# Kernel optimization log

Hardware: AMD Instinct MI355X
Metric: run time of the kernel (lower is better)

The kernel has to match this reference:

```python
import jax, jax.numpy as jnp
import numpy as np

RADIUS = 2  # kernel_size=5 -> r = (5-1)//2
EPS = 1e-8


def _diff(x, r, axis):
    # sliding-window sum from a cumsum along `axis` (same trick as BoxFilter.diff_x/diff_y)
    def sl(a, b):
        idx = [slice(None)] * x.ndim
        idx[axis] = slice(a, b)
        return x[tuple(idx)]
    left = sl(r, 2 * r + 1)
    middle = sl(2 * r + 1, None) - sl(None, -2 * r - 1)
    right = sl(-1, None) - sl(-2 * r - 1, -r - 1)
    return jnp.concatenate([left, middle, right], axis=axis)


def box_filter(x, r):
    # cumsum over H then window-diff, cumsum over W then window-diff
    return _diff(_diff(jnp.cumsum(x, axis=2), r, 2).cumsum(axis=3), r, 3)


def resize_bilinear_align_corners(x, out_h, out_w):
    # x: [N, C, h, w] -> [N, C, out_h, out_w], align_corners=True
    n, c, h, w = x.shape
    ys = jnp.linspace(0.0, h - 1.0, out_h, dtype=x.dtype)
    xs = jnp.linspace(0.0, w - 1.0, out_w, dtype=x.dtype)
    y0 = jnp.floor(ys).astype(jnp.int32)
    x0 = jnp.floor(xs).astype(jnp.int32)
    y1 = jnp.minimum(y0 + 1, h - 1)
    x1 = jnp.minimum(x0 + 1, w - 1)
    wy = (ys - y0.astype(x.dtype))[None, None, :, None]
    wx = (xs - x0.astype(x.dtype))[None, None, None, :]
    rows = x[:, :, y0, :] * (1 - wy) + x[:, :, y1, :] * wy  # [N,C,out_h,w]
    out = rows[:, :, :, x0] * (1 - wx) + rows[:, :, :, x1] * wx
    return out


def setup_inputs() -> dict:
    key = jax.random.key(0)
    k1, k2, k3 = jax.random.split(key, 3)
    return {
        "input_lowres": jax.random.uniform(k1, (8, 3, 256, 256), dtype=jnp.float32),
        "guide_lowres": jax.random.uniform(k2, (8, 3, 256, 256), dtype=jnp.float32),
        "input_highres": jax.random.uniform(k3, (8, 3, 1024, 1024), dtype=jnp.float32),
    }


def reference(input_lowres, guide_lowres, input_highres):
    x_lr, y_lr, x_hr = input_lowres, guide_lowres, input_highres
    r = RADIUS
    _, _, h_lr, w_lr = x_lr.shape
    _, _, h_hr, w_hr = x_hr.shape
    N = box_filter(jnp.ones((1, 1, h_lr, w_lr), dtype=x_lr.dtype), r)  # window pixel counts
    mean_x = box_filter(x_lr, r) / N
    mean_y = box_filter(y_lr, r) / N
    cov_xy = box_filter(x_lr * y_lr, r) / N - mean_x * mean_y
    var_x = box_filter(x_lr * x_lr, r) / N - mean_x * mean_x
    A = cov_xy / (var_x + EPS)
    b = mean_y - A * mean_x
    mean_A = resize_bilinear_align_corners(A, h_hr, w_hr)
    mean_b = resize_bilinear_align_corners(b, h_hr, w_hr)
    return mean_A * x_hr + mean_b
```

## Files before the change

kernel.cpp:

```cpp
#include <hip/hip_runtime.h>


typedef float f4 __attribute__((ext_vector_type(4)));

constexpr int H_LR = 256, W_LR = 256;
constexpr int H_HR = 1024, W_HR = 1024;
constexpr int NC   = 24;
constexpr int RAD  = 2;
constexpr int RPB  = 8;

constexpr int CS_W      = W_LR + 4;
constexpr int LDS_BYTES = 4 * CS_W * 4 * 4;

__global__ void __launch_bounds__(256) fgf_fused(const float* __restrict__ xlr,
                                                 const float* __restrict__ ylr,
                                                 const float* __restrict__ xhr,
                                                 float* __restrict__ out) {
    __shared__ __align__(16) char lds[LDS_BYTES];
    auto sx = reinterpret_cast<float(*)[W_LR]>(lds);
    auto sy = reinterpret_cast<float(*)[W_LR]>(lds + 8 * W_LR * 4);
    auto cs = reinterpret_cast<float(*)[CS_W][4]>(lds);
    auto ab = reinterpret_cast<float(*)[W_LR][2]>(lds);

    const int c  = blockIdx.y;
    const int i0 = blockIdx.x * RPB;
    const int t  = (int)threadIdx.x;
    const float scale = (float)(H_LR - 1) / (float)(H_HR - 1);

    const int y0min = (int)((float)i0 * scale);

    const int lrbase = c * (H_LR * W_LR);
    f4 stx[2], sty[2];
    int lr_[2], q_[2];
    #pragma unroll
    for (int half = 0; half < 2; ++half) {
        const int idx = half * 256 + t;
        lr_[half] = idx >> 6;
        q_[half]  = idx & 63;
        const int gr = y0min - 2 + lr_[half];
        f4 vx = {0.f, 0.f, 0.f, 0.f};
        f4 vy = {0.f, 0.f, 0.f, 0.f};
        if (gr >= 0 && gr < H_LR) {
            vx = *(const f4*)(xlr + lrbase + gr * W_LR + q_[half] * 4);
            vy = *(const f4*)(ylr + lrbase + gr * W_LR + q_[half] * 4);
        }
        stx[half] = vx;
        sty[half] = vy;
    }
    const size_t hrbase = ((size_t)c << 20) + (size_t)i0 * W_HR + t * 4;
    f4 xv[RPB];
    #pragma unroll
    for (int k = 0; k < RPB; ++k)
        xv[k] = *(const f4*)(xhr + hrbase + (size_t)k * W_HR);

    #pragma unroll
    for (int half = 0; half < 2; ++half) {
        *(f4*)&sx[lr_[half]][q_[half] * 4] = stx[half];
        *(f4*)&sy[lr_[half]][q_[half] * 4] = sty[half];
    }
    __syncthreads();

    float vx[8], vy[8];
    #pragma unroll
    for (int l = 0; l < 8; ++l) { vx[l] = sx[l][t]; vy[l] = sy[l][t]; }
    __syncthreads();

    #pragma unroll
    for (int rr = 0; rr < 4; ++rr) {
        float a = 0.f, b = 0.f, cxy = 0.f, cxx = 0.f;
        #pragma unroll
        for (int l = rr; l < rr + 5; ++l) {
            a += vx[l]; b += vy[l]; cxy += vx[l] * vy[l]; cxx += vx[l] * vx[l];
        }
        f4 v = {a, b, cxy, cxx};
        *(f4*)&cs[rr][t + 2][0] = v;
    }
    if (t < 2) {
        const f4 z = {0.f, 0.f, 0.f, 0.f};
        #pragma unroll
        for (int rr = 0; rr < 4; ++rr) {
            *(f4*)&cs[rr][t][0] = z;
            *(f4*)&cs[rr][t + W_LR + 2][0] = z;
        }
    }
    __syncthreads();

    const int hcnt = min(t + RAD, W_LR - 1) - max(t - RAD, 0) + 1;
    float aa[4], bb[4];
    #pragma unroll
    for (int rr = 0; rr < 4; ++rr) {
        f4 s = {0.f, 0.f, 0.f, 0.f};
        #pragma unroll
        for (int d = 0; d < 5; ++d) s += *(const f4*)&cs[rr][t + d][0];
        const int r  = y0min + rr;
        const int v0 = max(r - RAD, 0), v1 = min(r + RAD, H_LR - 1);
        const float inv = 1.0f / (float)((v1 - v0 + 1) * hcnt);
        const float mx  = s.x * inv;
        const float my  = s.y * inv;
        const float cov = s.z * inv - mx * my;
        const float var = s.w * inv - mx * mx;
        aa[rr] = cov / (var + 1e-8f);
        bb[rr] = my - aa[rr] * mx;
    }
    __syncthreads();

    #pragma unroll
    for (int rr = 0; rr < 4; ++rr) {
        ab[rr][t][0] = aa[rr];
        ab[rr][t][1] = bb[rr];
    }
    __syncthreads();

    float ax[4][4], bx[4][4];
    #pragma unroll
    for (int m = 0; m < 4; ++m) {
        const int   j   = t * 4 + m;
        const float fx  = (float)j * scale;
        const int   x0  = (int)fx;
        const float wx  = fx - (float)x0;
        const int   x1  = min(x0 + 1, W_LR - 1);
        const float wx0 = 1.f - wx;
        #pragma unroll
        for (int rr = 0; rr < 4; ++rr) {
            ax[rr][m] = ab[rr][x0][0] * wx0 + ab[rr][x1][0] * wx;
            bx[rr][m] = ab[rr][x0][1] * wx0 + ab[rr][x1][1] * wx;
        }
    }

    #pragma unroll
    for (int k = 0; k < RPB; ++k) {
        const int   i   = i0 + k;
        const float fy  = (float)i * scale;
        const int   yy0 = (int)fy;
        const float wy  = fy - (float)yy0;
        const int   l0  = yy0 - y0min;
        const int   l1  = min(yy0 + 1, H_LR - 1) - y0min;
        const float w0  = (l0 == 0 ? 1.f - wy : 0.f) + (l1 == 0 ? wy : 0.f);
        const float w1  = (l0 == 1 ? 1.f - wy : 0.f) + (l1 == 1 ? wy : 0.f);
        const float w2  = (l0 == 2 ? 1.f - wy : 0.f) + (l1 == 2 ? wy : 0.f);
        const float w3  = (l1 == 3 ? wy : 0.f);

        f4 ov;
        #pragma unroll
        for (int m = 0; m < 4; ++m) {
            const float a = ax[0][m] * w0 + ax[1][m] * w1 + ax[2][m] * w2 + ax[3][m] * w3;
            const float b = bx[0][m] * w0 + bx[1][m] * w1 + bx[2][m] * w2 + bx[3][m] * w3;
            ov[m] = a * xv[k][m] + b;
        }
        __builtin_nontemporal_store(ov, (f4*)(out + hrbase + (size_t)k * W_HR));
    }
}

extern "C" void kernel_launch(void* const* d_in, const int* in_sizes, int n_in,
                              void* d_out, int out_size, void* d_ws, size_t ws_size,
                              hipStream_t stream) {
    const float* x_lr = (const float*)d_in[0];
    const float* y_lr = (const float*)d_in[1];
    const float* x_hr = (const float*)d_in[2];
    float* out = (float*)d_out;

    dim3 grid(H_HR / RPB, NC, 1);
    fgf_fused<<<grid, 256, 0, stream>>>(x_lr, y_lr, x_hr, out);
}
```

Baseline: 41.93 us.

## Double rows per block, use sliding vertical sums, and software-pipeline high-res loads

Each block now produces 16 high-res rows from 6 low-res coefficient rows, halving the grid and cutting redundant low-res staging and box-filter work per output row. Vertical box sums use a running add/subtract window. Horizontal interpolation reads only three neighbouring A/b coefficients per thread instead of gathering per output column. High-res input loads go through a 4-deep rolling register buffer rather than all being loaded up front. The risk is fewer blocks for latency hiding and more register pressure from the larger per-thread coefficient arrays.

```diff
diff --git a/kernel.cpp b/kernel.cpp
--- a/kernel.cpp
+++ b/kernel.cpp
@@ -2,15 +2,18 @@
 
 
 typedef float f4 __attribute__((ext_vector_type(4)));
+typedef float f2 __attribute__((ext_vector_type(2)));
 
 constexpr int H_LR = 256, W_LR = 256;
 constexpr int H_HR = 1024, W_HR = 1024;
 constexpr int NC   = 24;
 constexpr int RAD  = 2;
-constexpr int RPB  = 8;
+constexpr int RPB  = 16;
+constexpr int NAB  = 6;
+constexpr int NST  = 10;
+constexpr int CS_W = W_LR + 4;
 
-constexpr int CS_W      = W_LR + 4;
-constexpr int LDS_BYTES = 4 * CS_W * 4 * 4;
+constexpr int LDS_BYTES = NAB * CS_W * 4 * 4;
 
 __global__ void __launch_bounds__(256) fgf_fused(const float* __restrict__ xlr,
                                                  const float* __restrict__ ylr,
@@ -18,9 +21,9 @@
                                                  float* __restrict__ out) {
     __shared__ __align__(16) char lds[LDS_BYTES];
     auto sx = reinterpret_cast<float(*)[W_LR]>(lds);
-    auto sy = reinterpret_cast<float(*)[W_LR]>(lds + 8 * W_LR * 4);
+    auto sy = reinterpret_cast<float(*)[W_LR]>(lds + NST * W_LR * 4);
     auto cs = reinterpret_cast<float(*)[CS_W][4]>(lds);
-    auto ab = reinterpret_cast<float(*)[W_LR][2]>(lds);
+    auto ab = reinterpret_cast<f2(*)[W_LR]>(lds);
 
     const int c  = blockIdx.y;
     const int i0 = blockIdx.x * RPB;
@@ -30,55 +33,54 @@
     const int y0min = (int)((float)i0 * scale);
 
     const int lrbase = c * (H_LR * W_LR);
-    f4 stx[2], sty[2];
-    int lr_[2], q_[2];
+    f4  stv[5];
+    int soff[5];
     #pragma unroll
-    for (int half = 0; half < 2; ++half) {
-        const int idx = half * 256 + t;
-        lr_[half] = idx >> 6;
-        q_[half]  = idx & 63;
-        const int gr = y0min - 2 + lr_[half];
-        f4 vx = {0.f, 0.f, 0.f, 0.f};
-        f4 vy = {0.f, 0.f, 0.f, 0.f};
-        if (gr >= 0 && gr < H_LR) {
-            vx = *(const f4*)(xlr + lrbase + gr * W_LR + q_[half] * 4);
-            vy = *(const f4*)(ylr + lrbase + gr * W_LR + q_[half] * 4);
-        }
-        stx[half] = vx;
-        sty[half] = vy;
+    for (int r = 0; r < 5; ++r) {
+        const int  idx = r * 256 + t;
+        const bool isx = idx < NST * 64;
+        const int  id2 = isx ? idx : idx - NST * 64;
+        const int  lr  = id2 >> 6, q = id2 & 63;
+        const int  gr  = y0min - 2 + lr;
+        const float* src = isx ? xlr : ylr;
+        f4 v = {0.f, 0.f, 0.f, 0.f};
+        if (gr >= 0 && gr < H_LR) v = *(const f4*)(src + lrbase + gr * W_LR + q * 4);
+        stv[r]  = v;
+        soff[r] = (isx ? 0 : NST * W_LR) + lr * W_LR + q * 4;
     }
-    const size_t hrbase = ((size_t)c << 20) + (size_t)i0 * W_HR + t * 4;
-    f4 xv[RPB];
-    #pragma unroll
-    for (int k = 0; k < RPB; ++k)
-        xv[k] = *(const f4*)(xhr + hrbase + (size_t)k * W_HR);
-
-    #pragma unroll
-    for (int half = 0; half < 2; ++half) {
-        *(f4*)&sx[lr_[half]][q_[half] * 4] = stx[half];
-        *(f4*)&sy[lr_[half]][q_[half] * 4] = sty[half];
+    {
+        float* base = (float*)lds;
+        #pragma unroll
+        for (int r = 0; r < 5; ++r) *(f4*)(base + soff[r]) = stv[r];
     }
     __syncthreads();
 
-    float vx[8], vy[8];
+    float vx[NST], vy[NST];
     #pragma unroll
-    for (int l = 0; l < 8; ++l) { vx[l] = sx[l][t]; vy[l] = sy[l][t]; }
+    for (int l = 0; l < NST; ++l) { vx[l] = sx[l][t]; vy[l] = sy[l][t]; }
     __syncthreads();
 
+    float pxy[NST], pxx[NST];
     #pragma unroll
-    for (int rr = 0; rr < 4; ++rr) {
-        float a = 0.f, b = 0.f, cxy = 0.f, cxx = 0.f;
-        #pragma unroll
-        for (int l = rr; l < rr + 5; ++l) {
-            a += vx[l]; b += vy[l]; cxy += vx[l] * vy[l]; cxx += vx[l] * vx[l];
+    for (int l = 0; l < NST; ++l) { pxy[l] = vx[l] * vy[l]; pxx[l] = vx[l] * vx[l]; }
+    float s0 = 0.f, s1 = 0.f, s2 = 0.f, s3 = 0.f;
+    #pragma unroll
+    for (int l = 0; l < 5; ++l) { s0 += vx[l]; s1 += vy[l]; s2 += pxy[l]; s3 += pxx[l]; }
+    #pragma unroll
+    for (int rr = 0; rr < NAB; ++rr) {
+        const f4 v = {s0, s1, s2, s3};
+        *(f4*)&cs[rr][t + 2][0] = v;
+        if (rr + 1 < NAB) {
+            s0 += vx[rr + 5] - vx[rr];
+            s1 += vy[rr + 5] - vy[rr];
+            s2 += pxy[rr + 5] - pxy[rr];
+            s3 += pxx[rr + 5] - pxx[rr];
         }
-        f4 v = {a, b, cxy, cxx};
-        *(f4*)&cs[rr][t + 2][0] = v;
     }
     if (t < 2) {
         const f4 z = {0.f, 0.f, 0.f, 0.f};
         #pragma unroll
-        for (int rr = 0; rr < 4; ++rr) {
+        for (int rr = 0; rr < NAB; ++rr) {
             *(f4*)&cs[rr][t][0] = z;
             *(f4*)&cs[rr][t + W_LR + 2][0] = z;
         }
@@ -86,9 +88,9 @@
     __syncthreads();
 
     const int hcnt = min(t + RAD, W_LR - 1) - max(t - RAD, 0) + 1;
-    float aa[4], bb[4];
+    float aa[NAB], bb[NAB];
     #pragma unroll
-    for (int rr = 0; rr < 4; ++rr) {
+    for (int rr = 0; rr < NAB; ++rr) {
         f4 s = {0.f, 0.f, 0.f, 0.f};
         #pragma unroll
         for (int d = 0; d < 5; ++d) s += *(const f4*)&cs[rr][t + d][0];
@@ -105,47 +107,73 @@
     __syncthreads();
 
     #pragma unroll
-    for (int rr = 0; rr < 4; ++rr) {
-        ab[rr][t][0] = aa[rr];
-        ab[rr][t][1] = bb[rr];
-    }
+    for (int rr = 0; rr < NAB; ++rr) ab[rr][t] = f2{aa[rr], bb[rr]};
     __syncthreads();
 
-    float ax[4][4], bx[4][4];
+    const int cl = max(t - 1, 0), ch = min(t + 1, W_LR - 1);
+    f2 A3[NAB][3];
+    #pragma unroll
+    for (int rr = 0; rr < NAB; ++rr) {
+        A3[rr][0] = ab[rr][cl];
+        A3[rr][1] = ab[rr][t];
+        A3[rr][2] = ab[rr][ch];
+    }
+
+    float wxv[4];
+    bool  lo[4], hi[4];
     #pragma unroll
     for (int m = 0; m < 4; ++m) {
-        const int   j   = t * 4 + m;
-        const float fx  = (float)j * scale;
-        const int   x0  = (int)fx;
-        const float wx  = fx - (float)x0;
-        const int   x1  = min(x0 + 1, W_LR - 1);
-        const float wx0 = 1.f - wx;
-        #pragma unroll
-        for (int rr = 0; rr < 4; ++rr) {
-            ax[rr][m] = ab[rr][x0][0] * wx0 + ab[rr][x1][0] * wx;
-            bx[rr][m] = ab[rr][x0][1] * wx0 + ab[rr][x1][1] * wx;
-        }
+        const int   j  = t * 4 + m;
+        const float fx = (float)j * scale;
+        const int   x0 = (int)fx;
+        wxv[m] = fx - (float)x0;
+        lo[m]  = (x0 < t);
+        hi[m]  = (x0 == t) && (t < W_LR - 1);
     }
+
+    const size_t hrbase = ((size_t)c << 20) + (size_t)i0 * W_HR + t * 4;
+    f4 buf0 = *(const f4*)(xhr + hrbase);
+    f4 buf1 = *(const f4*)(xhr + hrbase + W_HR);
+    f4 buf2 = *(const f4*)(xhr + hrbase + 2 * (size_t)W_HR);
+    f4 buf3 = *(const f4*)(xhr + hrbase + 3 * (size_t)W_HR);
 
     #pragma unroll
     for (int k = 0; k < RPB; ++k) {
-        const int   i   = i0 + k;
-        const float fy  = (float)i * scale;
+        f4 xvk;
+        if ((k & 3) == 0) xvk = buf0;
+        else if ((k & 3) == 1) xvk = buf1;
+        else if ((k & 3) == 2) xvk = buf2;
+        else xvk = buf3;
+        if (k + 4 < RPB) {
+            const f4 nv = *(const f4*)(xhr + hrbase + (size_t)(k + 4) * W_HR);
+            if ((k & 3) == 0) buf0 = nv;
+            else if ((k & 3) == 1) buf1 = nv;
+            else if ((k & 3) == 2) buf2 = nv;
+            else buf3 = nv;
+        }
+
+        const float fy  = (float)(i0 + k) * scale;
         const int   yy0 = (int)fy;
         const float wy  = fy - (float)yy0;
         const int   l0  = yy0 - y0min;
         const int   l1  = min(yy0 + 1, H_LR - 1) - y0min;
-        const float w0  = (l0 == 0 ? 1.f - wy : 0.f) + (l1 == 0 ? wy : 0.f);
-        const float w1  = (l0 == 1 ? 1.f - wy : 0.f) + (l1 == 1 ? wy : 0.f);
-        const float w2  = (l0 == 2 ? 1.f - wy : 0.f) + (l1 == 2 ? wy : 0.f);
-        const float w3  = (l1 == 3 ? wy : 0.f);
+        f2 r0 = {0.f, 0.f}, r1 = {0.f, 0.f}, r2 = {0.f, 0.f};
+        #pragma unroll
+        for (int rr = 0; rr < NAB; ++rr) {
+            const float w = (l0 == rr ? 1.f - wy : 0.f) + (l1 == rr ? wy : 0.f);
+            r0 += w * A3[rr][0];
+            r1 += w * A3[rr][1];
+            r2 += w * A3[rr][2];
+        }
 
         f4 ov;
         #pragma unroll
         for (int m = 0; m < 4; ++m) {
-            const float a = ax[0][m] * w0 + ax[1][m] * w1 + ax[2][m] * w2 + ax[3][m] * w3;
-            const float b = bx[0][m] * w0 + bx[1][m] * w1 + bx[2][m] * w2 + bx[3][m] * w3;
-            ov[m] = a * xv[k][m] + b;
+            const f2 pl = lo[m] ? r0 : r1;
+            const f2 ph = hi[m] ? r2 : r1;
+            const float a = pl.x * (1.f - wxv[m]) + ph.x * wxv[m];
+            const float b = pl.y * (1.f - wxv[m]) + ph.y * wxv[m];
+            ov[m] = a * xvk[m] + b;
         }
         __builtin_nontemporal_store(ov, (f4*)(out + hrbase + (size_t)k * W_HR));
     }
```

Measured after the change: 42.03 us. Within noise of the previous version (+0.3%).
